# Kernel optimization log

Hardware: AMD Instinct MI355X
Metric: run time of the kernel (lower is better)

Reference implementation:

```python
import jax, jax.numpy as jnp
import numpy as np

N = 1024      # num nodes
E = 16384     # num edges
P = 8192      # num query pairs
HD1 = 64      # hidden_dim_1
HD2 = 64      # hidden_dim_2
VOCAB = 1000  # max_x + 1
EPS = 1e-5


def gcn_conv(x, W, b, src, dst, n):
    # PyG GCNConv: h = D^{-1/2} (A + I) D^{-1/2} (x @ W) + b
    h = x @ W
    loop = jnp.arange(n)
    s = jnp.concatenate([src, loop])
    d = jnp.concatenate([dst, loop])
    deg = jnp.zeros((n,), h.dtype).at[d].add(1.0)
    dis = jax.lax.rsqrt(deg)  # deg >= 1 due to self-loops
    norm = dis[s] * dis[d]
    out = jnp.zeros_like(h).at[d].add(norm[:, None] * h[s])
    return out + b


def graph_norm(x, w, b, alpha):
    # PyG GraphNorm with a single graph: stats over node dim (axis 0)
    mean = jnp.mean(x, axis=0, keepdims=True)
    sh = x - alpha * mean
    var = jnp.mean(sh * sh, axis=0, keepdims=True)
    return w * sh / jnp.sqrt(var + EPS) + b


def _forward(x_ids, ei, pos, emb, gW0, gb0, gnw0, gnb0, gna0, gW1, gb1,
             gnw1, gnb1, gna1, m1W, m1b, m2W, m2b, m3W, m3b,
             gn3w, gn3b, gn3a, ldW, ldb):
    n = x_ids.shape[0]
    src, dst = ei[0], ei[1]
    x = emb[x_ids]                                            # [n, HD1]
    # 1-WL: two GCNConv -> GraphNorm -> ReLU blocks
    x = jax.nn.relu(graph_norm(gcn_conv(x, gW0, gb0, src, dst, n), gnw0, gnb0, gna0))
    x = jax.nn.relu(graph_norm(gcn_conv(x, gW1, gb1, src, dst, n), gnw1, gnb1, gna1))
    # O(n^2) outer product: X[i,j] = x[i] * x[j]
    X = x[:, None, :] * x[None, :, :]                         # [n, n, HD1]
    eim = jnp.zeros((n, n), x.dtype).at[src, dst].set(1.0)    # adjacency indicator
    # add_chan = eye(n) @ eim = eim
    X = jnp.concatenate([X, eim[:, :, None]], axis=-1)        # [n, n, HD1+1]
    # 2-FWL refinement (layer2 = 1)
    x1 = jax.nn.relu(X @ m1W + m1b)                           # [n, n, HD2]
    x2 = jax.nn.relu(X @ m2W + m2b)                           # [n, n, HD2]
    prod = jnp.einsum('ikc,kjc->ijc', x1, x2)                 # per-channel bmm
    X = jnp.concatenate([X, prod], axis=-1)                   # [n, n, HD1+1+HD2]
    X = jax.nn.relu(graph_norm(X @ m3W + m3b, gn3w, gn3b, gn3a))
    # symmetric mul-pool then gather query pairs
    X = X * jnp.transpose(X, (1, 0, 2))                       # [n, n, HD2]
    feat = X[pos[:, 0], pos[:, 1]]                            # [P, HD2]
    return feat @ ldW + ldb                                   # [P, 1]


def setup_inputs() -> dict:
    key = jax.random.key(0)
    ks = jax.random.split(key, 12)
    sc = lambda k, s: jax.random.normal(k, s, jnp.float32) * 0.05
    d = {}
    d['x_ids'] = jax.random.randint(ks[0], (N,), 0, VOCAB)
    d['ei'] = jax.random.randint(ks[1], (2, E), 0, N)
    d['pos'] = jax.random.randint(ks[2], (P, 2), 0, N)
    d['emb'] = sc(ks[3], (VOCAB, HD1))
    d['gW0'] = sc(ks[4], (HD1, HD1)); d['gb0'] = jnp.zeros((HD1,), jnp.float32)
    d['gnw0'] = jnp.ones((HD1,), jnp.float32); d['gnb0'] = jnp.zeros((HD1,), jnp.float32); d['gna0'] = jnp.ones((HD1,), jnp.float32)
    d['gW1'] = sc(ks[5], (HD1, HD1)); d['gb1'] = jnp.zeros((HD1,), jnp.float32)
    d['gnw1'] = jnp.ones((HD1,), jnp.float32); d['gnb1'] = jnp.zeros((HD1,), jnp.float32); d['gna1'] = jnp.ones((HD1,), jnp.float32)
    d['m1W'] = sc(ks[6], (HD1 + 1, HD2)); d['m1b'] = jnp.zeros((HD2,), jnp.float32)
    d['m2W'] = sc(ks[7], (HD1 + 1, HD2)); d['m2b'] = jnp.zeros((HD2,), jnp.float32)
    d['m3W'] = sc(ks[8], (HD2 + HD1 + 1, HD2)); d['m3b'] = jnp.zeros((HD2,), jnp.float32)
    d['gn3w'] = jnp.ones((HD2,), jnp.float32); d['gn3b'] = jnp.zeros((HD2,), jnp.float32); d['gn3a'] = jnp.ones((HD2,), jnp.float32)
    d['ldW'] = sc(ks[9], (HD2, 1)); d['ldb'] = jnp.zeros((1,), jnp.float32)
    return d


def reference(x_ids, ei, pos, emb, gW0, gb0, gnw0, gnb0, gna0, gW1, gb1,
              gnw1, gnb1, gna1, m1W, m1b, m2W, m2b, m3W, m3b,
              gn3w, gn3b, gn3a, ldW, ldb):
    return _forward(x_ids, ei, pos, emb, gW0, gb0, gnw0, gnb0, gna0, gW1, gb1,
                    gnw1, gnb1, gna1, m1W, m1b, m2W, m2b, m3W, m3b,
                    gn3w, gn3b, gn3a, ldW, ldb)
```

## Files before the change

### kernel.cpp

```cpp
#include <hip/hip_runtime.h>


typedef unsigned short u16;
typedef unsigned int u32;

#define DI static __device__ __forceinline__

DI float bf2f(u16 u) { union { u32 i; float f; } v; v.i = ((u32)u) << 16; return v.f; }
DI u16 f2bf(float f) {
  union { float f; u32 i; } v; v.f = f;
  u32 u = v.i;
  return (u16)((u + 0x7fffu + ((u >> 16) & 1u)) >> 16);
}

typedef __bf16 bf16x8 __attribute__((ext_vector_type(8)));
typedef float f32x4 __attribute__((ext_vector_type(4)));

#define MFMA16(a, b, c) __builtin_amdgcn_mfma_f32_16x16x32_bf16((a), (b), (c), 0, 0, 0)

typedef const __attribute__((address_space(1))) u32* gas1;
typedef __attribute__((address_space(3))) u32* las3;


__global__ void k_setup(const int* __restrict__ xids, const float* __restrict__ emb,
                        float* __restrict__ xf, float* __restrict__ deg,
                        u32* __restrict__ eimu) {
  int g = blockIdx.x * 256 + threadIdx.x;
  if (g < 262144) eimu[g] = 0u;
  if (g < 1024) deg[g] = 1.0f;
  if (g < 65536) {
    int i = g >> 6, d = g & 63;
    xf[g] = emb[xids[i] * 64 + d];
  }
}

__global__ void k_edges(const int* __restrict__ ei, float* __restrict__ deg,
                        unsigned char* __restrict__ eim) {
  int e = blockIdx.x * 256 + threadIdx.x;
  if (e < 16384) {
    int s = ei[e], d = ei[16384 + e];
    atomicAdd(&deg[d], 1.0f);
    eim[s * 1024 + d] = 1;
  }
}

__global__ void k_gemm_node(const float* __restrict__ xf, const float* __restrict__ W,
                            const float* __restrict__ gb, const float* __restrict__ deg,
                            float* __restrict__ h, float* __restrict__ agg) {
  __shared__ float xrow[64];
  int i = blockIdx.x, c = threadIdx.x;
  xrow[c] = xf[i * 64 + c];
  __syncthreads();
  float s = 0.f;
#pragma unroll
  for (int d = 0; d < 64; ++d) s += xrow[d] * W[d * 64 + c];
  h[i * 64 + c] = s;
  agg[i * 64 + c] = s / deg[i] + gb[c];
}

__global__ void k_agg(const int* __restrict__ ei, const float* __restrict__ deg,
                      const float* __restrict__ h, float* __restrict__ agg) {
  int g = blockIdx.x * 256 + threadIdx.x;
  int e = g >> 6, c = g & 63;
  int s = ei[e], d = ei[16384 + e];
  float nrm = rsqrtf(deg[s]) * rsqrtf(deg[d]);
  atomicAdd(&agg[d * 64 + c], nrm * h[s * 64 + c]);
}

__global__ void k_gnorm(const float* __restrict__ agg, const float* __restrict__ gw,
                        const float* __restrict__ gbb, const float* __restrict__ ga,
                        float* __restrict__ xf, u16* __restrict__ xb, int last) {
  int c = blockIdx.x, t = threadIdx.x;
  float s = 0.f, ss = 0.f;
  for (int i = t; i < 1024; i += 256) {
    float v = agg[i * 64 + c];
    s += v; ss += v * v;
  }
  __shared__ float Ls[256], Lss[256];
  Ls[t] = s; Lss[t] = ss;
  __syncthreads();
  for (int off = 128; off > 0; off >>= 1) {
    if (t < off) { Ls[t] += Ls[t + off]; Lss[t] += Lss[t + off]; }
    __syncthreads();
  }
  float m = Ls[0] * (1.f / 1024.f);
  float a = ga[c];
  float var = Lss[0] * (1.f / 1024.f) - (2.f * a - a * a) * m * m;
  float sc = gw[c] * rsqrtf(fmaxf(var, 0.f) + 1e-5f);
  float bb = gbb[c];
  for (int i = t; i < 1024; i += 256) {
    float v = agg[i * 64 + c];
    float y = fmaxf(sc * (v - a * m) + bb, 0.f);
    xf[i * 64 + c] = y;
    if (last) xb[i * 64 + c] = f2bf(y);
  }
}

__global__ __launch_bounds__(256, 2) void k_build12(
    const u16* __restrict__ xbg, const unsigned char* __restrict__ eim,
    const float* __restrict__ m1W, const float* __restrict__ m1b,
    const float* __restrict__ m2W, const float* __restrict__ m2b,
    u16* __restrict__ x1tg, u16* __restrict__ x2tg, int cbase) {
  __shared__ u16 As[128 * 80];
  __shared__ u16 Bs[128 * 80];
  __shared__ u16 Cs[64 * 140];
  __shared__ unsigned char El[128 * 132];
  __shared__ float wsc[64];
  int b = blockIdx.x;
  int cg = b & 3;
  int rest = b >> 2;
  int which = rest >> 6;
  int t6 = rest & 63;
  int rbase = (t6 >> 3) * 128, sbase = (t6 & 7) * 128;
  const float* W = which ? m2W : m1W;
  const float* bias = which ? m2b : m1b;
  u16* outg = which ? x2tg : x1tg;
  int t = threadIdx.x;
  {
    int row = t >> 1, half = t & 1;
    const u32* gB = (const u32*)(xbg + (sbase + row) * 64 + half * 32);
    u32* dstB = (u32*)&Bs[row * 80 + half * 32];
#pragma unroll
    for (int k = 0; k < 16; ++k) dstB[k] = gB[k];
    int ab = which ? sbase : rbase;
    int bb = which ? rbase : sbase;
    const u32* gE = (const u32*)(eim + (size_t)(ab + row) * 1024 + bb + half * 64);
    u32* dstE = (u32*)&El[row * 132 + half * 64];
#pragma unroll
    for (int k = 0; k < 16; ++k) dstE[k] = gE[k];
  }
  int lane = t & 63, w = t >> 6;
  int q = lane >> 4, r = lane & 15;
  int wr = w >> 1, wc = w & 1;
  for (int ci = 0; ci < 4; ++ci) {
    int cl = cg * 4 + ci;
    int c = cbase + cl;
    if (t < 64) wsc[t] = W[t * 64 + c];
    __syncthreads();
    {
      int row = t >> 1, half = t & 1;
      const u32* ga = (const u32*)(xbg + (rbase + row) * 64 + half * 32);
      u32* dstA = (u32*)&As[row * 80 + half * 32];
#pragma unroll
      for (int k = 0; k < 16; ++k) {
        u32 u = ga[k];
        float f0 = bf2f((u16)(u & 0xffffu)) * wsc[half * 32 + 2 * k];
        float f1 = bf2f((u16)(u >> 16)) * wsc[half * 32 + 2 * k + 1];
        dstA[k] = (u32)f2bf(f0) | ((u32)f2bf(f1) << 16);
      }
    }
    __syncthreads();
    f32x4 z4 = {0.f, 0.f, 0.f, 0.f};
    f32x4 acc[4][4];
#pragma unroll
    for (int mi = 0; mi < 4; ++mi)
#pragma unroll
      for (int ni = 0; ni < 4; ++ni) acc[mi][ni] = z4;
#pragma unroll
    for (int ks = 0; ks < 2; ++ks) {
      bf16x8 af[4], bfr[4];
#pragma unroll
      for (int mi = 0; mi < 4; ++mi)
        af[mi] = *(const bf16x8*)&As[(wr * 64 + mi * 16 + r) * 80 + ks * 32 + q * 8];
#pragma unroll
      for (int ni = 0; ni < 4; ++ni)
        bfr[ni] = *(const bf16x8*)&Bs[(wc * 64 + ni * 16 + r) * 80 + ks * 32 + q * 8];
#pragma unroll
      for (int mi = 0; mi < 4; ++mi)
#pragma unroll
        for (int ni = 0; ni < 4; ++ni) acc[mi][ni] = MFMA16(af[mi], bfr[ni], acc[mi][ni]);
    }
    float w64 = W[64 * 64 + c];
    float bsv = bias[c];
#pragma unroll
    for (int mi = 0; mi < 4; ++mi) {
#pragma unroll
      for (int ni = 0; ni < 4; ++ni) {
        int col = wc * 64 + ni * 16 + r;
#pragma unroll
        for (int tt = 0; tt < 4; ++tt) {
          int row2 = wr * 64 + mi * 16 + q * 4 + tt;
          float e = (float)(which ? El[col * 132 + row2] : El[row2 * 132 + col]);
          acc[mi][ni][tt] = fmaxf(acc[mi][ni][tt] + e * w64 + bsv, 0.f);
        }
      }
    }
    u16* outp = outg + (size_t)cl * 1048576;
#pragma unroll
    for (int p = 0; p < 2; ++p) {
      __syncthreads();
      if (wr == p) {
#pragma unroll
        for (int mi = 0; mi < 4; ++mi)
#pragma unroll
          for (int ni = 0; ni < 4; ++ni) {
            int col = wc * 64 + ni * 16 + r;
#pragma unroll
            for (int tt = 0; tt < 4; ++tt) {
              int lrow = mi * 16 + q * 4 + tt;
              Cs[lrow * 140 + col] = f2bf(acc[mi][ni][tt]);
            }
          }
      }
      __syncthreads();
      {
        int rl = t >> 4, ch = t & 15;
#pragma unroll
        for (int it = 0; it < 4; ++it) {
          int row = it * 16 + rl;
          uint4 v = *(const uint4*)&Cs[row * 140 + ch * 8];
          *(uint4*)(outp + (size_t)(rbase + p * 64 + row) * 1024 + sbase + ch * 8) = v;
        }
      }
    }
  }
}

__global__ __launch_bounds__(256, 4) void k_prodgemm(
    const u16* __restrict__ x1tg, const u16* __restrict__ x2tg,
    u16* __restrict__ prod, int cbase) {
  __shared__ u16 pool[17408];
  int b = blockIdx.x;
  int cl = (b & 7) + ((b >> 9) << 3);
  int tile = (b >> 3) & 63;
  int i0 = (tile >> 3) * 128, j0 = (tile & 7) * 128;
  const u16* Ap = x1tg + (size_t)cl * 1048576;
  const u16* Bp = x2tg + (size_t)cl * 1048576;
  u16* Pp = prod + (size_t)(cbase + cl) * 1048576;
  int t = threadIdx.x, lane = t & 63, w = t >> 6;
  int q = lane >> 4, r = lane & 15;
  int wr = w >> 1, wc = w & 1;
  int lrow = lane >> 3, lcol = (lane & 7) * 8;
  f32x4 z4 = {0.f, 0.f, 0.f, 0.f};
  f32x4 acc[4][4];
#pragma unroll
  for (int mi = 0; mi < 4; ++mi)
#pragma unroll
    for (int ni = 0; ni < 4; ++ni) acc[mi][ni] = z4;
  for (int kk = 0; kk < 1024; kk += 64) {
    __syncthreads();
#pragma unroll
    for (int s8 = 0; s8 < 4; ++s8) {
      int rowbase = w * 32 + s8 * 8;
      int grow = rowbase + lrow;
      __builtin_amdgcn_global_load_lds(
          (gas1)(Ap + (size_t)(i0 + grow) * 1024 + kk + lcol),
          (las3)&pool[rowbase * 64], 16, 0, 0);
      __builtin_amdgcn_global_load_lds(
          (gas1)(Bp + (size_t)(j0 + grow) * 1024 + kk + lcol),
          (las3)&pool[8192 + rowbase * 64], 16, 0, 0);
    }
    __syncthreads();
#pragma unroll
    for (int ks = 0; ks < 2; ++ks) {
      bf16x8 af[4], bfr[4];
#pragma unroll
      for (int mi = 0; mi < 4; ++mi)
        af[mi] = *(const bf16x8*)&pool[(wr * 64 + mi * 16 + r) * 64 + ks * 32 + q * 8];
#pragma unroll
      for (int ni = 0; ni < 4; ++ni)
        bfr[ni] = *(const bf16x8*)&pool[8192 + (wc * 64 + ni * 16 + r) * 64 + ks * 32 + q * 8];
#pragma unroll
      for (int mi = 0; mi < 4; ++mi)
#pragma unroll
        for (int ni = 0; ni < 4; ++ni) acc[mi][ni] = MFMA16(af[mi], bfr[ni], acc[mi][ni]);
    }
  }
  __syncthreads();
#pragma unroll
  for (int mi = 0; mi < 4; ++mi)
#pragma unroll
    for (int ni = 0; ni < 4; ++ni) {
      int col = wc * 64 + ni * 16 + r;
#pragma unroll
      for (int tt = 0; tt < 4; ++tt) {
        int row2 = wr * 64 + mi * 16 + q * 4 + tt;
        pool[row2 * 136 + col] = f2bf(acc[mi][ni][tt]);
      }
    }
  __syncthreads();
  {
    int rseg = t >> 4, cseg = t & 15;
#pragma unroll
    for (int it = 0; it < 8; ++it) {
      int row = it * 16 + rseg;
      uint4 v = *(const uint4*)&pool[row * 136 + cseg * 8];
      *(uint4*)(Pp + (size_t)(i0 + row) * 1024 + j0 + cseg * 8) = v;
    }
  }
}

__global__ __launch_bounds__(256, 3) void k_buildT(
    const u16* __restrict__ xbg, const unsigned char* __restrict__ eim,
    u16* PT, const float* __restrict__ m3W, const float* __restrict__ m3b,
    float* __restrict__ S, float* __restrict__ SS) {
  __shared__ u16 A[64 * 136];
  __shared__ u16 Wt[64 * 136];
  __shared__ u16 scratch[64 * 66];
  __shared__ float xi[64];
  int i = blockIdx.x;
  int t = threadIdx.x, lane = t & 63, w = t >> 6;
  int q = lane >> 4, r = lane & 15;
  {
    int zidx = i * 256 + t;
    if (zidx < 65536) { S[zidx] = 0.f; SS[zidx] = 0.f; }
  }
  if (t < 64) xi[t] = bf2f(xbg[i * 64 + t]);
  {
    int row = t >> 1, half = t & 1;
    int rsrc = row < 64 ? row : row + 1;
    const float4* gw = (const float4*)(m3W + rsrc * 64 + half * 32);
#pragma unroll
    for (int k = 0; k < 8; ++k) {
      float4 f = gw[k];
      Wt[(half * 32 + 4 * k + 0) * 136 + row] = f2bf(f.x);
      Wt[(half * 32 + 4 * k + 1) * 136 + row] = f2bf(f.y);
      Wt[(half * 32 + 4 * k + 2) * 136 + row] = f2bf(f.z);
      Wt[(half * 32 + 4 * k + 3) * 136 + row] = f2bf(f.w);
    }
  }
  float w64c[4], b3c[4];
#pragma unroll
  for (int ni = 0; ni < 4; ++ni) {
    int cc = ni * 16 + r;
    w64c[ni] = m3W[64 * 64 + cc];
    b3c[ni] = m3b[cc];
  }
  for (int jc = 0; jc < 16; ++jc) {
    int j0 = jc * 64;
    __syncthreads();
    {
      int jj = t >> 2, quar = t & 3;
      const u32* gx = (const u32*)(xbg + (j0 + jj) * 64 + quar * 16);
      u32* dst = (u32*)&A[jj * 136 + quar * 16];
#pragma unroll
      for (int k = 0; k < 8; ++k) {
        u32 u = gx[k];
        float f0 = bf2f((u16)(u & 0xffffu)) * xi[quar * 16 + 2 * k];
        float f1 = bf2f((u16)(u >> 16)) * xi[quar * 16 + 2 * k + 1];
        dst[k] = (u32)f2bf(f0) | ((u32)f2bf(f1) << 16);
      }
      int p = t >> 2, pt = t & 3;
      const uint4* gp = (const uint4*)(PT + (size_t)p * 1048576 + (size_t)i * 1024 + j0 + pt * 16);
      uint4 v0 = gp[0];
      uint2 v1 = ((const uint2*)gp)[2];
      uint2 v2 = ((const uint2*)gp)[3];
      u32* sw = (u32*)&scratch[p * 66 + pt * 16];
      sw[0] = v0.x; sw[1] = v0.y; sw[2] = v0.z; sw[3] = v0.w;
      sw[4] = v1.x; sw[5] = v1.y; sw[6] = v2.x; sw[7] = v2.y;
    }
    __syncthreads();
    {
#pragma unroll
      for (int jj2 = 0; jj2 < 8; ++jj2) {
        int jr = w * 16 + jj2 * 2;
        u32 two = *(const u32*)&scratch[lane * 66 + jr];
        A[jr * 136 + 64 + lane] = (u16)(two & 0xffffu);
        A[(jr + 1) * 136 + 64 + lane] = (u16)(two >> 16);
      }
    }
    __syncthreads();
    f32x4 z4 = {0.f, 0.f, 0.f, 0.f};
    f32x4 acc[4];
#pragma unroll
    for (int ni = 0; ni < 4; ++ni) acc[ni] = z4;
#pragma unroll
    for (int ks = 0; ks < 4; ++ks) {
      bf16x8 af, bfr[4];
      af = *(const bf16x8*)&A[(w * 16 + r) * 136 + ks * 32 + q * 8];
#pragma unroll
      for (int ni = 0; ni < 4; ++ni)
        bfr[ni] = *(const bf16x8*)&Wt[(ni * 16 + r) * 136 + ks * 32 + q * 8];
#pragma unroll
      for (int ni = 0; ni < 4; ++ni) acc[ni] = MFMA16(af, bfr[ni], acc[ni]);
    }
#pragma unroll
    for (int tt = 0; tt < 4; ++tt) {
      int jj = w * 16 + q * 4 + tt;
      float ev = (float)eim[(size_t)i * 1024 + j0 + jj];
#pragma unroll
      for (int ni = 0; ni < 4; ++ni)
        acc[ni][tt] = acc[ni][tt] + ev * w64c[ni] + b3c[ni];
    }
    __syncthreads();
#pragma unroll
    for (int ni = 0; ni < 4; ++ni) {
      int cc = ni * 16 + r;
#pragma unroll
      for (int tt = 0; tt < 4; ++tt) {
        int jj = w * 16 + q * 4 + tt;
        A[cc * 136 + jj] = f2bf(acc[ni][tt]);
      }
    }
    __syncthreads();
    {
      int pl = t >> 3, off = (t & 7) * 8;
#pragma unroll
      for (int k = 0; k < 2; ++k) {
        int plane = k * 32 + pl;
        uint4 v = *(const uint4*)&A[plane * 136 + off];
        *(uint4*)(PT + (size_t)plane * 1048576 + (size_t)i * 1024 + j0 + off) = v;
      }
    }
  }
}

__global__ void k_stats(const u16* __restrict__ Tg, float* __restrict__ S,
                        float* __restrict__ SS) {
  int b = blockIdx.x;
  int c = b >> 3, ic = b & 7;
  int t = threadIdx.x;
  const u16* base = Tg + (size_t)c * 1048576 + (size_t)ic * 131072 + t * 4;
  float s0 = 0.f, s1 = 0.f, s2 = 0.f, s3 = 0.f;
  float q0 = 0.f, q1 = 0.f, q2 = 0.f, q3 = 0.f;
  for (int ii = 0; ii < 128; ++ii) {
    uint2 u = *(const uint2*)(base + (size_t)ii * 1024);
    float v0 = bf2f((u16)(u.x & 0xffffu)), v1 = bf2f((u16)(u.x >> 16));
    float v2 = bf2f((u16)(u.y & 0xffffu)), v3 = bf2f((u16)(u.y >> 16));
    s0 += v0; q0 += v0 * v0;
    s1 += v1; q1 += v1 * v1;
    s2 += v2; q2 += v2 * v2;
    s3 += v3; q3 += v3 * v3;
  }
  int base2 = c * 1024 + t * 4;
  atomicAdd(&S[base2 + 0], s0);
  atomicAdd(&S[base2 + 1], s1);
  atomicAdd(&S[base2 + 2], s2);
  atomicAdd(&S[base2 + 3], s3);
  atomicAdd(&SS[base2 + 0], q0);
  atomicAdd(&SS[base2 + 1], q1);
  atomicAdd(&SS[base2 + 2], q2);
  atomicAdd(&SS[base2 + 3], q3);
}

__global__ void k_statsfin(const float* __restrict__ S, const float* __restrict__ SS,
                           const float* __restrict__ gn3w, const float* __restrict__ gn3b,
                           const float* __restrict__ gn3a,
                           float* __restrict__ normA, float* __restrict__ normB) {
  int idx = blockIdx.x * 256 + threadIdx.x;
  int c = idx & 63, j = idx >> 6;
  float sum = S[c * 1024 + j];
  float ssum = SS[c * 1024 + j];
  float m = sum * (1.f / 1024.f);
  float a = gn3a[c];
  float var = ssum * (1.f / 1024.f) - (2.f * a - a * a) * m * m;
  float sc = gn3w[c] * rsqrtf(fmaxf(var, 0.f) + 1e-5f);
  normA[idx] = sc;
  normB[idx] = gn3b[c] - sc * a * m;
}

__global__ void k_final(const u16* __restrict__ Tg, const float* __restrict__ normA,
                        const float* __restrict__ normB, const int* __restrict__ pos,
                        const float* __restrict__ ldW, const float* __restrict__ ldb,
                        float* __restrict__ out) {
  int t = threadIdx.x, w = t >> 6, lane = t & 63;
  int p = blockIdx.x * 4 + w;
  int i = pos[2 * p], j = pos[2 * p + 1];
  float t1 = bf2f(Tg[(size_t)lane * 1048576 + (size_t)i * 1024 + j]);
  float y1 = fmaxf(normA[j * 64 + lane] * t1 + normB[j * 64 + lane], 0.f);
  float t2 = bf2f(Tg[(size_t)lane * 1048576 + (size_t)j * 1024 + i]);
  float y2 = fmaxf(normA[i * 64 + lane] * t2 + normB[i * 64 + lane], 0.f);
  float z = y1 * y2 * ldW[lane];
#pragma unroll
  for (int off = 32; off > 0; off >>= 1) z += __shfl_down(z, off, 64);
  if (lane == 0) out[p] = z + ldb[0];
}

extern "C" void kernel_launch(void* const* d_in, const int* in_sizes, int n_in,
                              void* d_out, int out_size, void* d_ws, size_t ws_size,
                              hipStream_t stream) {
  const int* xids   = (const int*)d_in[0];
  const int* ei     = (const int*)d_in[1];
  const int* pos    = (const int*)d_in[2];
  const float* emb  = (const float*)d_in[3];
  const float* gW0  = (const float*)d_in[4];
  const float* gb0  = (const float*)d_in[5];
  const float* gnw0 = (const float*)d_in[6];
  const float* gnb0 = (const float*)d_in[7];
  const float* gna0 = (const float*)d_in[8];
  const float* gW1  = (const float*)d_in[9];
  const float* gb1  = (const float*)d_in[10];
  const float* gnw1 = (const float*)d_in[11];
  const float* gnb1 = (const float*)d_in[12];
  const float* gna1 = (const float*)d_in[13];
  const float* m1W  = (const float*)d_in[14];
  const float* m1b  = (const float*)d_in[15];
  const float* m2W  = (const float*)d_in[16];
  const float* m2b  = (const float*)d_in[17];
  const float* m3W  = (const float*)d_in[18];
  const float* m3b  = (const float*)d_in[19];
  const float* gn3w = (const float*)d_in[20];
  const float* gn3b = (const float*)d_in[21];
  const float* gn3a = (const float*)d_in[22];
  const float* ldW  = (const float*)d_in[23];
  const float* ldb  = (const float*)d_in[24];

  char* ws = (char*)d_ws;
  float* xf   = (float*)(ws + 0);
  float* h    = (float*)(ws + 262144);
  float* agg  = (float*)(ws + 524288);
  float* deg  = (float*)(ws + 786432);
  u16*   xb   = (u16*)(ws + 790528);
  unsigned char* eim = (unsigned char*)(ws + 921600);
  float* normA = (float*)(ws + 1970176);
  float* normB = (float*)(ws + 2232320);
  u16* x1tg = (u16*)(ws + 2494464);
  u16* x2tg = (u16*)(ws + 36048896);
  u16* prod = (u16*)(ws + 69603328);
  float* Sp  = (float*)x1tg;
  float* SSp = Sp + 65536;
  float* out = (float*)d_out;

  k_setup<<<1024, 256, 0, stream>>>(xids, emb, xf, deg, (u32*)eim);
  k_edges<<<64, 256, 0, stream>>>(ei, deg, eim);
  k_gemm_node<<<1024, 64, 0, stream>>>(xf, gW0, gb0, deg, h, agg);
  k_agg<<<4096, 256, 0, stream>>>(ei, deg, h, agg);
  k_gnorm<<<64, 256, 0, stream>>>(agg, gnw0, gnb0, gna0, xf, xb, 0);
  k_gemm_node<<<1024, 64, 0, stream>>>(xf, gW1, gb1, deg, h, agg);
  k_agg<<<4096, 256, 0, stream>>>(ei, deg, h, agg);
  k_gnorm<<<64, 256, 0, stream>>>(agg, gnw1, gnb1, gna1, xf, xb, 1);
  for (int g = 0; g < 4; ++g) {
    k_build12<<<512, 256, 0, stream>>>(xb, eim, m1W, m1b, m2W, m2b, x1tg, x2tg, g * 16);
    k_prodgemm<<<1024, 256, 0, stream>>>(x1tg, x2tg, prod, g * 16);
  }
  k_buildT<<<1024, 256, 0, stream>>>(xb, eim, prod, m3W, m3b, Sp, SSp);
  k_stats<<<512, 256, 0, stream>>>(prod, Sp, SSp);
  k_statsfin<<<256, 256, 0, stream>>>(Sp, SSp, gn3w, gn3b, gn3a, normA, normB);
  k_final<<<2048, 256, 0, stream>>>(prod, normA, normB, pos, ldW, ldb, out);
}
```

Measured before the change: 518.7 us.

## Software-pipeline buildT loads and stores across j-chunks with a separate staging buffer

Restructures the k_buildT loop so the global loads of the next 64-column chunk (PT slice and x rows) are issued into registers before the current chunk's compute. The output tile is written to a new staging buffer and stored to global one iteration later, which removes two barriers per iteration. Barriers become raw s_barrier plus an lgkmcnt wait, so outstanding global loads are not drained at each barrier. The eim row is cached in LDS once per block. In exchange it uses more LDS and registers, which may reduce occupancy under launch_bounds(256,3), and it depends on the in-place PT read-before-write ordering staying correct.

```diff
diff --git a/kernel.cpp b/kernel.cpp
--- a/kernel.cpp
+++ b/kernel.cpp
@@ -297,6 +297,8 @@
   __shared__ u16 A[64 * 136];
   __shared__ u16 Wt[64 * 136];
   __shared__ u16 scratch[64 * 66];
+  __shared__ u16 stg[64 * 72];
+  __shared__ unsigned char eimrow[1024];
   __shared__ float xi[64];
   int i = blockIdx.x;
   int t = threadIdx.x, lane = t & 63, w = t >> 6;
@@ -306,6 +308,7 @@
     if (zidx < 65536) { S[zidx] = 0.f; SS[zidx] = 0.f; }
   }
   if (t < 64) xi[t] = bf2f(xbg[i * 64 + t]);
+  ((u32*)eimrow)[t] = ((const u32*)(eim + (size_t)i * 1024))[t];
   {
     int row = t >> 1, half = t & 1;
     int rsrc = row < 64 ? row : row + 1;
@@ -326,40 +329,61 @@
     w64c[ni] = m3W[64 * 64 + cc];
     b3c[ni] = m3b[cc];
   }
+  int p4 = t >> 2, q4 = t & 3;
+  uint4 pva, pvb, xva, xvb;
+  {
+    const uint4* gp = (const uint4*)(PT + (size_t)p4 * 1048576 + (size_t)i * 1024 + q4 * 16);
+    pva = gp[0]; pvb = gp[1];
+    const uint4* gx = (const uint4*)(xbg + p4 * 64 + q4 * 16);
+    xva = gx[0]; xvb = gx[1];
+  }
   for (int jc = 0; jc < 16; ++jc) {
     int j0 = jc * 64;
-    __syncthreads();
+    asm volatile("s_waitcnt lgkmcnt(0)" ::: "memory");
+    __builtin_amdgcn_s_barrier();
+    asm volatile("" ::: "memory");
     {
-      int jj = t >> 2, quar = t & 3;
-      const u32* gx = (const u32*)(xbg + (j0 + jj) * 64 + quar * 16);
-      u32* dst = (u32*)&A[jj * 136 + quar * 16];
+      u32* sw = (u32*)&scratch[p4 * 66 + q4 * 16];
+      sw[0] = pva.x; sw[1] = pva.y; sw[2] = pva.z; sw[3] = pva.w;
+      sw[4] = pvb.x; sw[5] = pvb.y; sw[6] = pvb.z; sw[7] = pvb.w;
+      u32 xv[8] = {xva.x, xva.y, xva.z, xva.w, xvb.x, xvb.y, xvb.z, xvb.w};
+      u32* dst = (u32*)&A[p4 * 136 + q4 * 16];
 #pragma unroll
       for (int k = 0; k < 8; ++k) {
-        u32 u = gx[k];
-        float f0 = bf2f((u16)(u & 0xffffu)) * xi[quar * 16 + 2 * k];
-        float f1 = bf2f((u16)(u >> 16)) * xi[quar * 16 + 2 * k + 1];
+        u32 u = xv[k];
+        float f0 = bf2f((u16)(u & 0xffffu)) * xi[q4 * 16 + 2 * k];
+        float f1 = bf2f((u16)(u >> 16)) * xi[q4 * 16 + 2 * k + 1];
         dst[k] = (u32)f2bf(f0) | ((u32)f2bf(f1) << 16);
       }
-      int p = t >> 2, pt = t & 3;
-      const uint4* gp = (const uint4*)(PT + (size_t)p * 1048576 + (size_t)i * 1024 + j0 + pt * 16);
-      uint4 v0 = gp[0];
-      uint2 v1 = ((const uint2*)gp)[2];
-      uint2 v2 = ((const uint2*)gp)[3];
-      u32* sw = (u32*)&scratch[p * 66 + pt * 16];
-      sw[0] = v0.x; sw[1] = v0.y; sw[2] = v0.z; sw[3] = v0.w;
-      sw[4] = v1.x; sw[5] = v1.y; sw[6] = v2.x; sw[7] = v2.y;
-    }
-    __syncthreads();
-    {
-#pragma unroll
-      for (int jj2 = 0; jj2 < 8; ++jj2) {
-        int jr = w * 16 + jj2 * 2;
-        u32 two = *(const u32*)&scratch[lane * 66 + jr];
-        A[jr * 136 + 64 + lane] = (u16)(two & 0xffffu);
-        A[(jr + 1) * 136 + 64 + lane] = (u16)(two >> 16);
-      }
-    }
-    __syncthreads();
+    }
+    if (jc < 15) {
+      const uint4* gp = (const uint4*)(PT + (size_t)p4 * 1048576 + (size_t)i * 1024 + (j0 + 64) + q4 * 16);
+      pva = gp[0]; pvb = gp[1];
+      const uint4* gx = (const uint4*)(xbg + (j0 + 64 + p4) * 64 + q4 * 16);
+      xva = gx[0]; xvb = gx[1];
+    }
+    if (jc > 0) {
+      int pl = t >> 3, off = (t & 7) * 8;
+#pragma unroll
+      for (int k = 0; k < 2; ++k) {
+        int plane = k * 32 + pl;
+        uint4 v = *(const uint4*)&stg[plane * 72 + off];
+        *(uint4*)(PT + (size_t)plane * 1048576 + (size_t)i * 1024 + (j0 - 64) + off) = v;
+      }
+    }
+    asm volatile("s_waitcnt lgkmcnt(0)" ::: "memory");
+    __builtin_amdgcn_s_barrier();
+    asm volatile("" ::: "memory");
+#pragma unroll
+    for (int jj2 = 0; jj2 < 8; ++jj2) {
+      int jr = w * 16 + jj2 * 2;
+      u32 two = *(const u32*)&scratch[lane * 66 + jr];
+      A[jr * 136 + 64 + lane] = (u16)(two & 0xffffu);
+      A[(jr + 1) * 136 + 64 + lane] = (u16)(two >> 16);
+    }
+    asm volatile("s_waitcnt lgkmcnt(0)" ::: "memory");
+    __builtin_amdgcn_s_barrier();
+    asm volatile("" ::: "memory");
     f32x4 z4 = {0.f, 0.f, 0.f, 0.f};
     f32x4 acc[4];
 #pragma unroll
@@ -377,30 +401,31 @@
 #pragma unroll
     for (int tt = 0; tt < 4; ++tt) {
       int jj = w * 16 + q * 4 + tt;
-      float ev = (float)eim[(size_t)i * 1024 + j0 + jj];
+      float ev = (float)eimrow[j0 + jj];
 #pragma unroll
       for (int ni = 0; ni < 4; ++ni)
         acc[ni][tt] = acc[ni][tt] + ev * w64c[ni] + b3c[ni];
     }
-    __syncthreads();
 #pragma unroll
     for (int ni = 0; ni < 4; ++ni) {
       int cc = ni * 16 + r;
 #pragma unroll
       for (int tt = 0; tt < 4; ++tt) {
         int jj = w * 16 + q * 4 + tt;
-        A[cc * 136 + jj] = f2bf(acc[ni][tt]);
-      }
-    }
-    __syncthreads();
-    {
-      int pl = t >> 3, off = (t & 7) * 8;
-#pragma unroll
-      for (int k = 0; k < 2; ++k) {
-        int plane = k * 32 + pl;
-        uint4 v = *(const uint4*)&A[plane * 136 + off];
-        *(uint4*)(PT + (size_t)plane * 1048576 + (size_t)i * 1024 + j0 + off) = v;
-      }
+        stg[cc * 72 + jj] = f2bf(acc[ni][tt]);
+      }
+    }
+  }
+  asm volatile("s_waitcnt lgkmcnt(0)" ::: "memory");
+  __builtin_amdgcn_s_barrier();
+  asm volatile("" ::: "memory");
+  {
+    int pl = t >> 3, off = (t & 7) * 8;
+#pragma unroll
+    for (int k = 0; k < 2; ++k) {
+      int plane = k * 32 + pl;
+      uint4 v = *(const uint4*)&stg[plane * 72 + off];
+      *(uint4*)(PT + (size_t)plane * 1048576 + (size_t)i * 1024 + 960 + off) = v;
     }
   }
 }
```

New measurement: 508.0 us. 2.1% less time.

## Pipeline k_buildT with register prefetch and direct accumulator stores

Applied to the files above, without the earlier changes.

Restructures k_buildT so that the PT and xbg tiles for the next chunk are prefetched into registers two chunks ahead. The m3W fragments are kept in registers across the loop, and the eim row is cached in LDS. The LDS scratch transpose and the LDS staging of the output are removed, so MFMA results go straight to global memory as 8-byte stores, and several barriers per iteration are dropped. In exchange, register pressure rises and the output stores become less coalesced (32-byte runs per plane instead of full rows).

```diff
diff --git a/kernel.cpp b/kernel.cpp
--- a/kernel.cpp
+++ b/kernel.cpp
@@ -294,18 +294,30 @@
     const u16* __restrict__ xbg, const unsigned char* __restrict__ eim,
     u16* PT, const float* __restrict__ m3W, const float* __restrict__ m3b,
     float* __restrict__ S, float* __restrict__ SS) {
-  __shared__ u16 A[64 * 136];
+  __shared__ u16 A[64 * 136 + 2560];
   __shared__ u16 Wt[64 * 136];
-  __shared__ u16 scratch[64 * 66];
+  __shared__ unsigned char eimrow[1024];
   __shared__ float xi[64];
   int i = blockIdx.x;
   int t = threadIdx.x, lane = t & 63, w = t >> 6;
   int q = lane >> 4, r = lane & 15;
+  int p4 = t >> 2, q4 = t & 3;
+
+  uint4 pvA[2], pvB[2], xvA[2], xvB[2];
+#pragma unroll
+  for (int m = 0; m < 2; ++m) {
+    const uint4* gp = (const uint4*)(PT + (size_t)p4 * 1048576 + (size_t)i * 1024 + m * 64 + q4 * 16);
+    pvA[m] = gp[0]; pvB[m] = gp[1];
+    const uint4* gx = (const uint4*)(xbg + (m * 64 + p4) * 64 + q4 * 16);
+    xvA[m] = gx[0]; xvB[m] = gx[1];
+  }
+
   {
     int zidx = i * 256 + t;
     if (zidx < 65536) { S[zidx] = 0.f; SS[zidx] = 0.f; }
   }
   if (t < 64) xi[t] = bf2f(xbg[i * 64 + t]);
+  ((u32*)eimrow)[t] = ((const u32*)(eim + (size_t)i * 1024))[t];
   {
     int row = t >> 1, half = t & 1;
     int rsrc = row < 64 ? row : row + 1;
@@ -326,81 +338,83 @@
     w64c[ni] = m3W[64 * 64 + cc];
     b3c[ni] = m3b[cc];
   }
+  asm volatile("s_waitcnt lgkmcnt(0)" ::: "memory");
+  __builtin_amdgcn_s_barrier();
+  asm volatile("" ::: "memory");
+  bf16x8 wreg[4][4];
+#pragma unroll
+  for (int ni = 0; ni < 4; ++ni)
+#pragma unroll
+    for (int ks = 0; ks < 4; ++ks)
+      wreg[ni][ks] = *(const bf16x8*)&Wt[(ni * 16 + r) * 136 + ks * 32 + q * 8];
+  float xiv[16];
+#pragma unroll
+  for (int k = 0; k < 16; ++k) xiv[k] = xi[q4 * 16 + k];
+
+#pragma unroll 2
   for (int jc = 0; jc < 16; ++jc) {
+    int s = jc & 1;
     int j0 = jc * 64;
-    __syncthreads();
+    asm volatile("s_waitcnt lgkmcnt(0)" ::: "memory");
+    __builtin_amdgcn_s_barrier();
+    asm volatile("" ::: "memory");
     {
-      int jj = t >> 2, quar = t & 3;
-      const u32* gx = (const u32*)(xbg + (j0 + jj) * 64 + quar * 16);
-      u32* dst = (u32*)&A[jj * 136 + quar * 16];
+      u32 xw[8] = {xvA[s].x, xvA[s].y, xvA[s].z, xvA[s].w,
+                   xvB[s].x, xvB[s].y, xvB[s].z, xvB[s].w};
+      u32 ow[8];
 #pragma unroll
       for (int k = 0; k < 8; ++k) {
-        u32 u = gx[k];
-        float f0 = bf2f((u16)(u & 0xffffu)) * xi[quar * 16 + 2 * k];
-        float f1 = bf2f((u16)(u >> 16)) * xi[quar * 16 + 2 * k + 1];
-        dst[k] = (u32)f2bf(f0) | ((u32)f2bf(f1) << 16);
-      }
-      int p = t >> 2, pt = t & 3;
-      const uint4* gp = (const uint4*)(PT + (size_t)p * 1048576 + (size_t)i * 1024 + j0 + pt * 16);
-      uint4 v0 = gp[0];
-      uint2 v1 = ((const uint2*)gp)[2];
-      uint2 v2 = ((const uint2*)gp)[3];
-      u32* sw = (u32*)&scratch[p * 66 + pt * 16];
-      sw[0] = v0.x; sw[1] = v0.y; sw[2] = v0.z; sw[3] = v0.w;
-      sw[4] = v1.x; sw[5] = v1.y; sw[6] = v2.x; sw[7] = v2.y;
-    }
-    __syncthreads();
+        u32 u = xw[k];
+        float f0 = bf2f((u16)(u & 0xffffu)) * xiv[2 * k];
+        float f1 = bf2f((u16)(u >> 16)) * xiv[2 * k + 1];
+        ow[k] = (u32)f2bf(f0) | ((u32)f2bf(f1) << 16);
+      }
+      uint4 lo4 = {ow[0], ow[1], ow[2], ow[3]};
+      uint4 hi4 = {ow[4], ow[5], ow[6], ow[7]};
+      *(uint4*)&A[p4 * 136 + q4 * 16] = lo4;
+      *(uint4*)&A[p4 * 136 + q4 * 16 + 8] = hi4;
+    }
     {
-#pragma unroll
-      for (int jj2 = 0; jj2 < 8; ++jj2) {
-        int jr = w * 16 + jj2 * 2;
-        u32 two = *(const u32*)&scratch[lane * 66 + jr];
-        A[jr * 136 + 64 + lane] = (u16)(two & 0xffffu);
-        A[(jr + 1) * 136 + 64 + lane] = (u16)(two >> 16);
-      }
-    }
-    __syncthreads();
+      u32 pw[8] = {pvA[s].x, pvA[s].y, pvA[s].z, pvA[s].w,
+                   pvB[s].x, pvB[s].y, pvB[s].z, pvB[s].w};
+#pragma unroll
+      for (int jj = 0; jj < 16; ++jj) {
+        u32 wv = pw[jj >> 1];
+        u16 e = (jj & 1) ? (u16)(wv >> 16) : (u16)(wv & 0xffffu);
+        A[(q4 * 16 + jj) * 136 + 64 + p4] = e;
+      }
+    }
+    if (jc <= 13) {
+      const uint4* gp = (const uint4*)(PT + (size_t)p4 * 1048576 + (size_t)i * 1024 + (j0 + 128) + q4 * 16);
+      pvA[s] = gp[0]; pvB[s] = gp[1];
+      const uint4* gx = (const uint4*)(xbg + (j0 + 128 + p4) * 64 + q4 * 16);
+      xvA[s] = gx[0]; xvB[s] = gx[1];
+    }
+    asm volatile("s_waitcnt lgkmcnt(0)" ::: "memory");
+    __builtin_amdgcn_s_barrier();
+    asm volatile("" ::: "memory");
     f32x4 z4 = {0.f, 0.f, 0.f, 0.f};
     f32x4 acc[4];
 #pragma unroll
     for (int ni = 0; ni < 4; ++ni) acc[ni] = z4;
 #pragma unroll
     for (int ks = 0; ks < 4; ++ks) {
-      bf16x8 af, bfr[4];
-      af = *(const bf16x8*)&A[(w * 16 + r) * 136 + ks * 32 + q * 8];
-#pragma unroll
-      for (int ni = 0; ni < 4; ++ni)
-        bfr[ni] = *(const bf16x8*)&Wt[(ni * 16 + r) * 136 + ks * 32 + q * 8];
-#pragma unroll
-      for (int ni = 0; ni < 4; ++ni) acc[ni] = MFMA16(af, bfr[ni], acc[ni]);
-    }
-#pragma unroll
-    for (int tt = 0; tt < 4; ++tt) {
-      int jj = w * 16 + q * 4 + tt;
-      float ev = (float)eim[(size_t)i * 1024 + j0 + jj];
-#pragma unroll
-      for (int ni = 0; ni < 4; ++ni)
+      bf16x8 af = *(const bf16x8*)&A[(w * 16 + r) * 136 + ks * 32 + q * 8];
+#pragma unroll
+      for (int ni = 0; ni < 4; ++ni) acc[ni] = MFMA16(af, wreg[ni][ks], acc[ni]);
+    }
+    u32 e4 = *(const u32*)&eimrow[j0 + w * 16 + q * 4];
+#pragma unroll
+    for (int ni = 0; ni < 4; ++ni) {
+#pragma unroll
+      for (int tt = 0; tt < 4; ++tt) {
+        float ev = (float)((e4 >> (8 * tt)) & 255u);
         acc[ni][tt] = acc[ni][tt] + ev * w64c[ni] + b3c[ni];
-    }
-    __syncthreads();
-#pragma unroll
-    for (int ni = 0; ni < 4; ++ni) {
-      int cc = ni * 16 + r;
-#pragma unroll
-      for (int tt = 0; tt < 4; ++tt) {
-        int jj = w * 16 + q * 4 + tt;
-        A[cc * 136 + jj] = f2bf(acc[ni][tt]);
-      }
-    }
-    __syncthreads();
-    {
-      int pl = t >> 3, off = (t & 7) * 8;
-#pragma unroll
-      for (int k = 0; k < 2; ++k) {
-        int plane = k * 32 + pl;
-        uint4 v = *(const uint4*)&A[plane * 136 + off];
-        *(uint4*)(PT + (size_t)plane * 1048576 + (size_t)i * 1024 + j0 + off) = v;
-      }
+      }
+      u32 lo = (u32)f2bf(acc[ni][0]) | ((u32)f2bf(acc[ni][1]) << 16);
+      u32 hi = (u32)f2bf(acc[ni][2]) | ((u32)f2bf(acc[ni][3]) << 16);
+      uint2 v = {lo, hi};
+      *(uint2*)(PT + (size_t)(ni * 16 + r) * 1048576 + (size_t)i * 1024 + j0 + w * 16 + q * 4) = v;
     }
   }
 }
```

Result: no change. 517.3 us (-0.3%).
